# Kernel optimization log

Measured on AMD Instinct MI355X. Metric: run time of the kernel, lower is better.

The kernel has to match this reference:

```python
import jax, jax.numpy as jnp
import numpy as np

THRESHOLD = 1.0
SLOPE = 25.0  # snntorch surrogate.fast_sigmoid default

@jax.custom_vjp
def spike_fn(x):
    # heaviside forward, fast_sigmoid surrogate backward
    return (x > 0).astype(x.dtype)

def _spike_fwd(x):
    return spike_fn(x), x

def _spike_bwd(x, g):
    return (g / (SLOPE * jnp.abs(x) + 1.0) ** 2,)

spike_fn.defvjp(_spike_fwd, _spike_bwd)


def setup_inputs() -> dict:
    key = jax.random.key(0)
    ks = jax.random.split(key, 8)
    B, D_IN, H0, H1 = 16384, 512, 1024, 512
    def linear_params(kw, kb, fan_in, fan_out):
        bound = 1.0 / np.sqrt(fan_in)
        w = jax.random.uniform(kw, (fan_out, fan_in), jnp.float32, -bound, bound)
        b = jax.random.uniform(kb, (fan_out,), jnp.float32, -bound, bound)
        return w, b
    w1, b1 = linear_params(ks[0], ks[1], D_IN, H0)
    w2, b2 = linear_params(ks[2], ks[3], H0, H1)
    w3, b3 = linear_params(ks[4], ks[5], H1, 1)
    data = jax.random.normal(ks[6], (B, D_IN), jnp.float32)
    return {"data": data, "w1": w1, "b1": b1, "w2": w2, "b2": b2,
            "w3": w3, "b3": b3, "time_steps": 8}


def reference(data, w1, b1, w2, b2, w3, b3, time_steps):
    # Effective betas: snntorch clamps beta to [0,1]. lif1 beta = units0 (=1024) -> 1.0 (source bug, replicated).
    beta1 = jnp.float32(1.0)
    beta2 = jnp.float32(0.95)
    # data is constant across time, so fc1 output is step-invariant
    cur1 = data @ w1.T + b1                      # [B, H0]
    B, H0 = cur1.shape
    H1 = w2.shape[0]
    mem1_0 = jnp.zeros((B, H0), cur1.dtype)
    mem2_0 = jnp.zeros((B, H1), cur1.dtype)

    def step(carry, _):
        mem1, mem2 = carry
        # snntorch Leaky (reset_mechanism='subtract'): reset detected on OLD mem, detached
        reset1 = jax.lax.stop_gradient((mem1 > THRESHOLD).astype(mem1.dtype))
        mem1 = beta1 * mem1 + cur1 - reset1 * THRESHOLD
        spk1 = spike_fn(mem1 - THRESHOLD)
        cur2 = spk1 @ w2.T + b2                  # [B, H1]
        reset2 = jax.lax.stop_gradient((mem2 > THRESHOLD).astype(mem2.dtype))
        mem2 = beta2 * mem2 + cur2 - reset2 * THRESHOLD
        spk2 = spike_fn(mem2 - THRESHOLD)
        cur3 = spk2 @ w3.T + b3                  # [B, 1]
        return (mem1, mem2), cur3

    _, cur3_seq = jax.lax.scan(step, (mem1_0, mem2_0), None, length=time_steps)
    return jnp.mean(cur3_seq, axis=0)            # [B, 1]
```

## Files before the change

### kernel.cpp

```cpp
#include <hip/hip_runtime.h>
#include <hip/hip_bf16.h>
#include <cstdint>
#include <cstddef>


#define NB 16384
#define DIN 512
#define NH0 1024
#define NH1 512

typedef float f32x4 __attribute__((ext_vector_type(4)));
typedef short bf16x8 __attribute__((ext_vector_type(8)));

#define WS_PAT   0u
#define WS_W2H   19922944u
#define WS_W2M   20971520u
#define WS_W2L   22020096u

__device__ inline uint16_t f2bf(float f) {
    __hip_bfloat16 h = __float2bfloat16(f);
    return *reinterpret_cast<uint16_t*>(&h);
}
__device__ inline float bf2f(uint16_t u) {
    __hip_bfloat16 h = *reinterpret_cast<__hip_bfloat16*>(&u);
    return __bfloat162float(h);
}

__global__ void init_out_kernel(float* __restrict__ out,
                                const float* __restrict__ b3, int n) {
    int i = blockIdx.x * blockDim.x + threadIdx.x;
    if (i < n) out[i] = b3[0];
}

__global__ __launch_bounds__(256) void split3_kernel(
    const float* __restrict__ src, uint16_t* __restrict__ h,
    uint16_t* __restrict__ m, uint16_t* __restrict__ l, int n)
{
    int i = (blockIdx.x * 256 + threadIdx.x) * 4;
    if (i >= n) return;
    float4 f = *(const float4*)(src + i);
    float fv[4] = {f.x, f.y, f.z, f.w};
    uint32_t hw[2], mw[2], lw[2];
    #pragma unroll
    for (int g = 0; g < 2; ++g) {
        uint16_t hh[2], mm[2], ll[2];
        #pragma unroll
        for (int e = 0; e < 2; ++e) {
            float a = fv[2 * g + e];
            uint16_t h0 = f2bf(a);
            float d = __fsub_rn(a, bf2f(h0));
            uint16_t m0 = f2bf(d);
            float e2 = __fsub_rn(d, bf2f(m0));
            uint16_t l0 = f2bf(e2);
            hh[e] = h0; mm[e] = m0; ll[e] = l0;
        }
        hw[g] = (uint32_t)hh[0] | ((uint32_t)hh[1] << 16);
        mw[g] = (uint32_t)mm[0] | ((uint32_t)mm[1] << 16);
        lw[g] = (uint32_t)ll[0] | ((uint32_t)ll[1] << 16);
    }
    *(uint2*)(h + i) = make_uint2(hw[0], hw[1]);
    *(uint2*)(m + i) = make_uint2(mw[0], mw[1]);
    *(uint2*)(l + i) = make_uint2(lw[0], lw[1]);
}

__global__ __launch_bounds__(512, 4) void gemm1_spike_kernel(
    const float* __restrict__ data, const float* __restrict__ w1,
    const float* __restrict__ b1, uint8_t* __restrict__ pat)
{
    __shared__ float As[128][68];
    __shared__ float Bs[128][68];
    const int tid = threadIdx.x;
    const int tx = tid & 31;
    const int ty = tid >> 5;
    const int i0 = blockIdx.x * 128, n0 = blockIdx.y * 128;

    float acc[8][4] = {};
    float4 pa[4], pb[4];

    #pragma unroll
    for (int rep = 0; rep < 4; ++rep) {
        int idx = tid + rep * 512;
        int row = idx >> 4, c4 = (idx & 15) * 4;
        pa[rep] = *(const float4*)(data + (size_t)(i0 + row) * DIN + c4);
        pb[rep] = *(const float4*)(w1 + (size_t)(n0 + row) * DIN + c4);
    }

    for (int kb = 0; kb < DIN; kb += 64) {
        #pragma unroll
        for (int rep = 0; rep < 4; ++rep) {
            int idx = tid + rep * 512;
            int row = idx >> 4, c4 = (idx & 15) * 4;
            *(float4*)(&As[row][c4]) = pa[rep];
            *(float4*)(&Bs[row][c4]) = pb[rep];
        }
        __syncthreads();
        if (kb + 64 < DIN) {
            #pragma unroll
            for (int rep = 0; rep < 4; ++rep) {
                int idx = tid + rep * 512;
                int row = idx >> 4, c4 = (idx & 15) * 4;
                pa[rep] = *(const float4*)(data + (size_t)(i0 + row) * DIN + kb + 64 + c4);
                pb[rep] = *(const float4*)(w1 + (size_t)(n0 + row) * DIN + kb + 64 + c4);
            }
        }
        #pragma unroll 2
        for (int k4 = 0; k4 < 16; ++k4) {
            float4 a4[8], b4[4];
            #pragma unroll
            for (int ii = 0; ii < 8; ++ii)
                a4[ii] = *(const float4*)(&As[ty + ii * 16][k4 * 4]);
            #pragma unroll
            for (int nn = 0; nn < 4; ++nn)
                b4[nn] = *(const float4*)(&Bs[tx + nn * 32][k4 * 4]);
            #pragma unroll
            for (int ii = 0; ii < 8; ++ii) {
                #pragma unroll
                for (int nn = 0; nn < 4; ++nn) {
                    acc[ii][nn] = fmaf(a4[ii].x, b4[nn].x, acc[ii][nn]);
                    acc[ii][nn] = fmaf(a4[ii].y, b4[nn].y, acc[ii][nn]);
                    acc[ii][nn] = fmaf(a4[ii].z, b4[nn].z, acc[ii][nn]);
                    acc[ii][nn] = fmaf(a4[ii].w, b4[nn].w, acc[ii][nn]);
                }
            }
        }
        __syncthreads();
    }

    #pragma unroll
    for (int ii = 0; ii < 8; ++ii) {
        const int i = i0 + ty + ii * 16;
        #pragma unroll
        for (int nn = 0; nn < 4; ++nn) {
            const int n = n0 + tx + nn * 32;
            float x = __fadd_rn(acc[ii][nn], b1[n]);
            float mem = 0.0f;
            unsigned p = 0;
            #pragma unroll
            for (int t = 0; t < 8; ++t) {
                bool reset = mem > 1.0f;
                float tmp = __fadd_rn(mem, x);
                mem = reset ? __fsub_rn(tmp, 1.0f) : tmp;
                p |= (mem > 1.0f ? 1u : 0u) << t;
            }
            pat[(size_t)(n >> 6) * (NB * 64) + (size_t)i * 64 + (n & 63)] = (uint8_t)p;
        }
    }
}

__global__ __launch_bounds__(256, 2) void gemm2_mfma_kernel(
    const uint8_t* __restrict__ pat,
    const uint16_t* __restrict__ w2h, const uint16_t* __restrict__ w2m,
    const uint16_t* __restrict__ w2l,
    const float* __restrict__ b2, const float* __restrict__ w3,
    float* __restrict__ out)
{
    __shared__ __align__(16) uint16_t Bh_[8192];
    __shared__ __align__(16) uint16_t Bm_[8192];
    __shared__ __align__(16) uint16_t Bl_[8192];
    __shared__ __align__(16) uint8_t  Ap_[8192];

    const int tid  = threadIdx.x;
    const int lane = tid & 63;
    const int wv   = tid >> 6;
    const int lr   = lane & 15;
    const int lg   = lane >> 4;
    const int i0   = blockIdx.x * 64, n0 = blockIdx.y * 64;

    f32x4 acc[8][4];
    #pragma unroll
    for (int t = 0; t < 8; ++t)
        #pragma unroll
        for (int nf = 0; nf < 4; ++nf)
            acc[t][nf] = (f32x4)(0.0f);

    const int srow = tid >> 2;
    const int scol = (tid & 3) * 16;
    const size_t wbase = (size_t)(n0 + srow) * NH0 + scol;
    const size_t pbase = (size_t)i0 * 64 + (size_t)tid * 16;
    const int nf_w  = srow >> 4, lr_w = srow & 15;
    const int ub0 = (((scol >> 5)       * 4 + nf_w) * 64 + ((scol >> 3) & 3)       * 16 + lr_w) * 8;
    const int ub1 = ((((scol + 8) >> 5) * 4 + nf_w) * 64 + (((scol + 8) >> 3) & 3) * 16 + lr_w) * 8;

    uint4 rh0, rh1, rm0, rm1, rl0, rl1, rp;

#define K2_LOAD(kt) do { \
        const size_t o = wbase + (size_t)(kt) * 64; \
        rh0 = *(const uint4*)(w2h + o); rh1 = *(const uint4*)(w2h + o + 8); \
        rm0 = *(const uint4*)(w2m + o); rm1 = *(const uint4*)(w2m + o + 8); \
        rl0 = *(const uint4*)(w2l + o); rl1 = *(const uint4*)(w2l + o + 8); \
        rp  = *(const uint4*)(pat + (size_t)(kt) * (NB * 64) + pbase); \
    } while (0)

#define K2_WRITE(nb) do { \
        *(uint4*)(Bh_ + (nb) * 4096 + ub0) = rh0; *(uint4*)(Bh_ + (nb) * 4096 + ub1) = rh1; \
        *(uint4*)(Bm_ + (nb) * 4096 + ub0) = rm0; *(uint4*)(Bm_ + (nb) * 4096 + ub1) = rm1; \
        *(uint4*)(Bl_ + (nb) * 4096 + ub0) = rl0; *(uint4*)(Bl_ + (nb) * 4096 + ub1) = rl1; \
        *(uint2*)(Ap_ + (nb) * 4096 + ub0) = make_uint2(rp.x, rp.y); \
        *(uint2*)(Ap_ + (nb) * 4096 + ub1) = make_uint2(rp.z, rp.w); \
    } while (0)

    K2_LOAD(0);
    K2_WRITE(0);

    int cur = 0;
    for (int kbi = 0; kbi < 16; ++kbi) {
        __syncthreads();
        if (kbi < 15) K2_LOAD(kbi + 1);

        #pragma unroll
        for (int s = 0; s < 2; ++s) {
            bf16x8 bh[4], bm[4], bl[4];
            #pragma unroll
            for (int nf = 0; nf < 4; ++nf) {
                const int fo = cur * 4096 + ((s * 4 + nf) * 64 + lane) * 8;
                bh[nf] = *(const bf16x8*)(Bh_ + fo);
                bm[nf] = *(const bf16x8*)(Bm_ + fo);
                bl[nf] = *(const bf16x8*)(Bl_ + fo);
            }
            const uint2 p8 = *(const uint2*)(Ap_ + cur * 4096 +
                                             ((s * 4 + wv) * 64 + lane) * 8);
            #pragma unroll
            for (int t = 0; t < 8; ++t) {
                uint32_t y0 = (p8.x >> t) & 0x01010101u;
                uint32_t y1 = (p8.y >> t) & 0x01010101u;
                uint32_t s0 = __builtin_amdgcn_perm(0u, y0, 0x01010000u) | 0x02000200u;
                uint32_t s1x = __builtin_amdgcn_perm(0u, y0, 0x03030202u) | 0x02000200u;
                uint32_t s2x = __builtin_amdgcn_perm(0u, y1, 0x01010000u) | 0x02000200u;
                uint32_t s3x = __builtin_amdgcn_perm(0u, y1, 0x03030202u) | 0x02000200u;
                union { uint4 u; bf16x8 v; } af;
                af.u = make_uint4(__builtin_amdgcn_perm(0u, 0x3F008000u, s0),
                                  __builtin_amdgcn_perm(0u, 0x3F008000u, s1x),
                                  __builtin_amdgcn_perm(0u, 0x3F008000u, s2x),
                                  __builtin_amdgcn_perm(0u, 0x3F008000u, s3x));
                #pragma unroll
                for (int nf = 0; nf < 4; ++nf) {
                    acc[t][nf] = __builtin_amdgcn_mfma_f32_16x16x32_bf16(
                        af.v, bh[nf], acc[t][nf], 0, 0, 0);
                    acc[t][nf] = __builtin_amdgcn_mfma_f32_16x16x32_bf16(
                        af.v, bm[nf], acc[t][nf], 0, 0, 0);
                    acc[t][nf] = __builtin_amdgcn_mfma_f32_16x16x32_bf16(
                        af.v, bl[nf], acc[t][nf], 0, 0, 0);
                }
            }
        }

        if (kbi < 15) K2_WRITE(cur ^ 1);
        cur ^= 1;
    }

    float rowsum[4] = {0.0f, 0.0f, 0.0f, 0.0f};
    #pragma unroll
    for (int nf = 0; nf < 4; ++nf) {
        const int n = n0 + nf * 16 + lr;
        const float b2n = b2[n];
        const float w3n = w3[n];
        #pragma unroll
        for (int r = 0; r < 4; ++r) {
            float mem = 0.0f;
            int pc = 0;
            #pragma unroll
            for (int t = 0; t < 8; ++t) {
                bool reset = mem > 1.0f;
                float x   = __fadd_rn(acc[t][nf][r], b2n);
                float tmp = __fadd_rn(__fmul_rn(0.95f, mem), x);
                mem = reset ? __fsub_rn(tmp, 1.0f) : tmp;
                pc += (mem > 1.0f) ? 1 : 0;
            }
            rowsum[r] = fmaf(w3n, (float)pc, rowsum[r]);
        }
    }
    #pragma unroll
    for (int r = 0; r < 4; ++r) {
        float s = rowsum[r];
        s += __shfl_xor(s, 1);
        s += __shfl_xor(s, 2);
        s += __shfl_xor(s, 4);
        s += __shfl_xor(s, 8);
        if (lr == 0)
            atomicAdd(&out[i0 + wv * 16 + lg * 4 + r], 0.125f * s);
    }
}

extern "C" void kernel_launch(void* const* d_in, const int* in_sizes, int n_in,
                              void* d_out, int out_size, void* d_ws, size_t ws_size,
                              hipStream_t stream) {
    const float* data = (const float*)d_in[0];
    const float* w1   = (const float*)d_in[1];
    const float* b1   = (const float*)d_in[2];
    const float* w2   = (const float*)d_in[3];
    const float* b2   = (const float*)d_in[4];
    const float* w3   = (const float*)d_in[5];
    const float* b3   = (const float*)d_in[6];
    float* out = (float*)d_out;

    char* ws = (char*)d_ws;
    uint8_t*  pat = (uint8_t*)(ws + WS_PAT);
    uint16_t* w2h = (uint16_t*)(ws + WS_W2H);
    uint16_t* w2m = (uint16_t*)(ws + WS_W2M);
    uint16_t* w2l = (uint16_t*)(ws + WS_W2L);

    init_out_kernel<<<(NB + 255) / 256, 256, 0, stream>>>(out, b3, NB);
    split3_kernel<<<(NH1 * NH0 / 4 + 255) / 256, 256, 0, stream>>>(w2, w2h, w2m, w2l, NH1 * NH0);
    gemm1_spike_kernel<<<dim3(NB / 128, NH0 / 128), 512, 0, stream>>>(data, w1, b1, pat);
    gemm2_mfma_kernel<<<dim3(NB / 64, NH1 / 64), 256, 0, stream>>>(pat, w2h, w2m, w2l, b2, w3, out);
}
```

Measured before the change: 636.0 us.

## Reorder MFMA chain to break accumulator dependencies and drop gemm1 register prefetch

```diff
diff --git a/kernel.cpp b/kernel.cpp
--- a/kernel.cpp
+++ b/kernel.cpp
@@ -75,34 +75,18 @@
     const int i0 = blockIdx.x * 128, n0 = blockIdx.y * 128;
 
     float acc[8][4] = {};
-    float4 pa[4], pb[4];
-
-    #pragma unroll
-    for (int rep = 0; rep < 4; ++rep) {
-        int idx = tid + rep * 512;
-        int row = idx >> 4, c4 = (idx & 15) * 4;
-        pa[rep] = *(const float4*)(data + (size_t)(i0 + row) * DIN + c4);
-        pb[rep] = *(const float4*)(w1 + (size_t)(n0 + row) * DIN + c4);
-    }
 
     for (int kb = 0; kb < DIN; kb += 64) {
         #pragma unroll
         for (int rep = 0; rep < 4; ++rep) {
             int idx = tid + rep * 512;
             int row = idx >> 4, c4 = (idx & 15) * 4;
-            *(float4*)(&As[row][c4]) = pa[rep];
-            *(float4*)(&Bs[row][c4]) = pb[rep];
+            *(float4*)(&As[row][c4]) =
+                *(const float4*)(data + (size_t)(i0 + row) * DIN + kb + c4);
+            *(float4*)(&Bs[row][c4]) =
+                *(const float4*)(w1 + (size_t)(n0 + row) * DIN + kb + c4);
         }
         __syncthreads();
-        if (kb + 64 < DIN) {
-            #pragma unroll
-            for (int rep = 0; rep < 4; ++rep) {
-                int idx = tid + rep * 512;
-                int row = idx >> 4, c4 = (idx & 15) * 4;
-                pa[rep] = *(const float4*)(data + (size_t)(i0 + row) * DIN + kb + 64 + c4);
-                pb[rep] = *(const float4*)(w1 + (size_t)(n0 + row) * DIN + kb + 64 + c4);
-            }
-        }
         #pragma unroll 2
         for (int k4 = 0; k4 < 16; ++k4) {
             float4 a4[8], b4[4];
@@ -199,6 +183,19 @@
         *(uint2*)(Ap_ + (nb) * 4096 + ub1) = make_uint2(rp.z, rp.w); \
     } while (0)
 
+#define K2_EXPAND(af, p8, t) do { \
+        uint32_t y0 = ((p8).x >> (t)) & 0x01010101u; \
+        uint32_t y1 = ((p8).y >> (t)) & 0x01010101u; \
+        uint32_t s0 = __builtin_amdgcn_perm(0u, y0, 0x01010000u) | 0x02000200u; \
+        uint32_t s1x = __builtin_amdgcn_perm(0u, y0, 0x03030202u) | 0x02000200u; \
+        uint32_t s2x = __builtin_amdgcn_perm(0u, y1, 0x01010000u) | 0x02000200u; \
+        uint32_t s3x = __builtin_amdgcn_perm(0u, y1, 0x03030202u) | 0x02000200u; \
+        (af).u = make_uint4(__builtin_amdgcn_perm(0u, 0x3F008000u, s0), \
+                            __builtin_amdgcn_perm(0u, 0x3F008000u, s1x), \
+                            __builtin_amdgcn_perm(0u, 0x3F008000u, s2x), \
+                            __builtin_amdgcn_perm(0u, 0x3F008000u, s3x)); \
+    } while (0)
+
     K2_LOAD(0);
     K2_WRITE(0);
 
@@ -220,27 +217,35 @@
             const uint2 p8 = *(const uint2*)(Ap_ + cur * 4096 +
                                              ((s * 4 + wv) * 64 + lane) * 8);
             #pragma unroll
-            for (int t = 0; t < 8; ++t) {
-                uint32_t y0 = (p8.x >> t) & 0x01010101u;
-                uint32_t y1 = (p8.y >> t) & 0x01010101u;
-                uint32_t s0 = __builtin_amdgcn_perm(0u, y0, 0x01010000u) | 0x02000200u;
-                uint32_t s1x = __builtin_amdgcn_perm(0u, y0, 0x03030202u) | 0x02000200u;
-                uint32_t s2x = __builtin_amdgcn_perm(0u, y1, 0x01010000u) | 0x02000200u;
-                uint32_t s3x = __builtin_amdgcn_perm(0u, y1, 0x03030202u) | 0x02000200u;
-                union { uint4 u; bf16x8 v; } af;
-                af.u = make_uint4(__builtin_amdgcn_perm(0u, 0x3F008000u, s0),
-                                  __builtin_amdgcn_perm(0u, 0x3F008000u, s1x),
-                                  __builtin_amdgcn_perm(0u, 0x3F008000u, s2x),
-                                  __builtin_amdgcn_perm(0u, 0x3F008000u, s3x));
-                #pragma unroll
-                for (int nf = 0; nf < 4; ++nf) {
-                    acc[t][nf] = __builtin_amdgcn_mfma_f32_16x16x32_bf16(
-                        af.v, bh[nf], acc[t][nf], 0, 0, 0);
-                    acc[t][nf] = __builtin_amdgcn_mfma_f32_16x16x32_bf16(
-                        af.v, bm[nf], acc[t][nf], 0, 0, 0);
-                    acc[t][nf] = __builtin_amdgcn_mfma_f32_16x16x32_bf16(
-                        af.v, bl[nf], acc[t][nf], 0, 0, 0);
-                }
+            for (int tp = 0; tp < 4; ++tp) {
+                const int t0 = tp * 2, t1 = tp * 2 + 1;
+                union { uint4 u; bf16x8 v; } af0, af1;
+                K2_EXPAND(af0, p8, t0);
+                K2_EXPAND(af1, p8, t1);
+                #pragma unroll
+                for (int nf = 0; nf < 4; ++nf)
+                    acc[t0][nf] = __builtin_amdgcn_mfma_f32_16x16x32_bf16(
+                        af0.v, bh[nf], acc[t0][nf], 0, 0, 0);
+                #pragma unroll
+                for (int nf = 0; nf < 4; ++nf)
+                    acc[t1][nf] = __builtin_amdgcn_mfma_f32_16x16x32_bf16(
+                        af1.v, bh[nf], acc[t1][nf], 0, 0, 0);
+                #pragma unroll
+                for (int nf = 0; nf < 4; ++nf)
+                    acc[t0][nf] = __builtin_amdgcn_mfma_f32_16x16x32_bf16(
+                        af0.v, bm[nf], acc[t0][nf], 0, 0, 0);
+                #pragma unroll
+                for (int nf = 0; nf < 4; ++nf)
+                    acc[t1][nf] = __builtin_amdgcn_mfma_f32_16x16x32_bf16(
+                        af1.v, bm[nf], acc[t1][nf], 0, 0, 0);
+                #pragma unroll
+                for (int nf = 0; nf < 4; ++nf)
+                    acc[t0][nf] = __builtin_amdgcn_mfma_f32_16x16x32_bf16(
+                        af0.v, bl[nf], acc[t0][nf], 0, 0, 0);
+                #pragma unroll
+                for (int nf = 0; nf < 4; ++nf)
+                    acc[t1][nf] = __builtin_amdgcn_mfma_f32_16x16x32_bf16(
+                        af1.v, bl[nf], acc[t1][nf], 0, 0, 0);
             }
         }
 
```

After: 549.6 us. 13.6% less time.
